# Kernel tuning notes

Measured on AMD Instinct MI355X. Metric: run time of the kernel, lower is better.

## Reference

```python
import jax, jax.numpy as jnp
import numpy as np

B, T, D, H = 1, 2049, 1024, 16
HD = D // H                      # head_dim = 64
MAX_SEQ = 1025
L = 2 * MAX_SEQ - 1              # = T (required by the module's relative shift)

def setup_inputs() -> dict:
    key = jax.random.key(0)
    ks = jax.random.split(key, 12)
    s = 0.02
    return {
        'q': jax.random.normal(ks[0], (B, T, D), dtype=jnp.float32),
        'k': jax.random.normal(ks[1], (B, T, D), dtype=jnp.float32),
        'v': jax.random.normal(ks[2], (B, T, D), dtype=jnp.float32),
        'mask': jnp.tril(jnp.ones((1, 1, T, T), dtype=jnp.int32)),  # causal
        'Wq_w': jax.random.normal(ks[3], (D, D), dtype=jnp.float32) * s,
        'Wq_b': jnp.zeros((D,), dtype=jnp.float32),
        'Wk_w': jax.random.normal(ks[4], (D, D), dtype=jnp.float32) * s,
        'Wk_b': jnp.zeros((D,), dtype=jnp.float32),
        'Wv_w': jax.random.normal(ks[5], (D, D), dtype=jnp.float32) * s,
        'Wv_b': jnp.zeros((D,), dtype=jnp.float32),
        'Er': jax.random.normal(ks[6], (L, HD), dtype=jnp.float32),
        'Wo_w': jax.random.normal(ks[7], (D, D), dtype=jnp.float32) * s,
        'Wo_b': jnp.zeros((D,), dtype=jnp.float32),
    }

def reference(q, k, v, mask, Wq_w, Wq_b, Wk_w, Wk_b, Wv_w, Wv_b, Er, Wo_w, Wo_b):
    b, t, d = q.shape
    def proj(x, w, bias):
        # nn.Linear: x @ W^T + b ; then (B,T,H,HD) -> (B,H,T,HD)
        return (x @ w.T + bias).reshape(b, t, H, HD).transpose(0, 2, 1, 3)
    qh = proj(q, Wq_w, Wq_b)
    kh = proj(k, Wk_w, Wk_b)
    vh = proj(v, Wv_w, Wv_b)
    scores = jnp.einsum('bhtd,bhsd->bhts', qh, kh)          # (B,H,T,T)
    QEr = jnp.einsum('bhtd,ld->bhtl', qh, Er)               # (B,H,T,L) with L == T
    # _relative_shift: pad a zero row on seq dim then drop first row ->
    # row i becomes QEr row i+1, last row zeros (faithful to torch code)
    rel = jnp.concatenate([QEr[:, :, 1:, :], jnp.zeros_like(QEr[:, :, :1, :])], axis=2)
    scores = scores + rel
    scores = jnp.where(mask[:, :, :t, :t] == 0, -jnp.inf, scores)
    attn = jax.nn.softmax(scores / (HD ** 0.5), axis=-1)
    ctx = jnp.einsum('bhts,bhsd->bthd', attn, vh).reshape(b, t, d)
    return ctx @ Wo_w.T + Wo_b
```

## Files before the change

### kernel.cpp

```cpp
#include <hip/hip_runtime.h>
#include <hip/hip_bf16.h>
#include <math.h>

constexpr int T_SEQ = 2049;
constexpr int D_MODEL = 1024;
constexpr int N_HEAD = 16;
constexpr int HEAD_DIM = 64;
constexpr int VT_STRIDE = 2112;
constexpr int T1_ROWS = 1152;

typedef __attribute__((ext_vector_type(8))) short short8;
typedef __attribute__((ext_vector_type(4))) short short4v;
typedef __attribute__((ext_vector_type(4))) float floatx4;

__device__ inline void load_lds16(const void* g, void* l) {
  __builtin_amdgcn_global_load_lds(
      (const __attribute__((address_space(1))) unsigned int*)g,
      (__attribute__((address_space(3))) unsigned int*)l, 16, 0, 0);
}

__device__ inline short8 cvt8_bf16(const float* p) {
  float4 a = *(const float4*)p, b = *(const float4*)(p + 4);
  __hip_bfloat16 t[8] = {__float2bfloat16(a.x), __float2bfloat16(a.y),
                         __float2bfloat16(a.z), __float2bfloat16(a.w),
                         __float2bfloat16(b.x), __float2bfloat16(b.y),
                         __float2bfloat16(b.z), __float2bfloat16(b.w)};
  return *(const short8*)t;
}

__device__ inline float bf2f(__hip_bfloat16 x) { return __bfloat162float(x); }

__global__ __launch_bounds__(256) void cast_all(
    const float* __restrict__ q, const float* __restrict__ k,
    const float* __restrict__ v, const float* __restrict__ wq,
    const float* __restrict__ wk, const float* __restrict__ wv,
    const float* __restrict__ wo, __hip_bfloat16* __restrict__ qo,
    __hip_bfloat16* __restrict__ ko, __hip_bfloat16* __restrict__ vo,
    __hip_bfloat16* __restrict__ wqo, __hip_bfloat16* __restrict__ wko,
    __hip_bfloat16* __restrict__ wvo, __hip_bfloat16* __restrict__ woo) {
  const int z = blockIdx.y;
  const float* in;
  __hip_bfloat16* out;
  int n;
  switch (z) {
    case 0: in = q; out = qo; n = T_SEQ * D_MODEL; break;
    case 1: in = k; out = ko; n = T_SEQ * D_MODEL; break;
    case 2: in = v; out = vo; n = T_SEQ * D_MODEL; break;
    case 3: in = wq; out = wqo; n = D_MODEL * D_MODEL; break;
    case 4: in = wk; out = wko; n = D_MODEL * D_MODEL; break;
    case 5: in = wv; out = wvo; n = D_MODEL * D_MODEL; break;
    default: in = wo; out = woo; n = D_MODEL * D_MODEL; break;
  }
  const int i = (blockIdx.x * 256 + threadIdx.x) * 8;
  if (i + 8 > n) return;
  *(short8*)(out + i) = cvt8_bf16(in + i);
}

template <int BN, int OUTK>
__global__ __launch_bounds__(256) void mfma_gemm(
    const __hip_bfloat16* __restrict__ A0, const __hip_bfloat16* __restrict__ A1,
    const __hip_bfloat16* __restrict__ A2, const __hip_bfloat16* __restrict__ W0,
    const __hip_bfloat16* __restrict__ W1, const __hip_bfloat16* __restrict__ W2,
    const float* __restrict__ bias0, const float* __restrict__ bias1,
    const float* __restrict__ bias2, void* C0, void* C1, void* C2, int M) {
  constexpr int K = D_MODEL;
  constexpr int NT = BN / 32;
  __shared__ __align__(16) __hip_bfloat16 As[128 * 64];
  __shared__ __align__(16) __hip_bfloat16 Bs[BN * 64];

  const int z = blockIdx.z;
  const short* A = (const short*)(z == 0 ? A0 : z == 1 ? A1 : A2);
  const short* W = (const short*)(z == 0 ? W0 : z == 1 ? W1 : W2);
  const float* bias = z == 0 ? bias0 : z == 1 ? bias1 : bias2;
  void* C = z == 0 ? C0 : z == 1 ? C1 : C2;

  const int tid = threadIdx.x;
  const int wave = tid >> 6, lane = tid & 63;
  const int col = lane & 15, quad = lane >> 4;
  const int wm = wave >> 1, wn = wave & 1;
  const int m0 = blockIdx.y * 128, n0 = blockIdx.x * BN;

  const int srow = lane >> 3;
  const int sslot = lane & 7;
  const int sch = sslot ^ srow;

  floatx4 acc[4][NT];
#pragma unroll
  for (int i = 0; i < 4; i++)
#pragma unroll
    for (int j = 0; j < NT; j++) acc[i][j] = (floatx4){0.f, 0.f, 0.f, 0.f};

  for (int k0 = 0; k0 < K; k0 += 64) {
    if (k0) __syncthreads();
#pragma unroll
    for (int i = 0; i < 4; i++) {
      const int rb = (wave * 4 + i) * 8;
      const int am = min(m0 + rb + srow, M - 1);
      load_lds16(A + (size_t)am * K + k0 + sch * 8, (char*)As + rb * 128);
    }
#pragma unroll
    for (int i = 0; i < BN / 32; i++) {
      const int rb = (wave * (BN / 32) + i) * 8;
      const int bn = n0 + rb + srow;
      load_lds16(W + (size_t)bn * K + k0 + sch * 8, (char*)Bs + rb * 128);
    }
    __syncthreads();

#pragma unroll
    for (int kk = 0; kk < 2; kk++) {
      short8 af[4], bf[NT];
#pragma unroll
      for (int t = 0; t < 4; t++) {
        const int ra = wm * 64 + t * 16 + col;
        af[t] = *(const short8*)(As + ra * 64 + ((kk * 4 + quad) ^ (ra & 7)) * 8);
      }
#pragma unroll
      for (int t = 0; t < NT; t++) {
        const int rb = wn * (BN / 2) + t * 16 + col;
        bf[t] = *(const short8*)(Bs + rb * 64 + ((kk * 4 + quad) ^ (rb & 7)) * 8);
      }
#pragma unroll
      for (int mt = 0; mt < 4; mt++)
#pragma unroll
        for (int nt = 0; nt < NT; nt++)
          acc[mt][nt] = __builtin_amdgcn_mfma_f32_16x16x32_bf16(af[mt], bf[nt],
                                                                acc[mt][nt], 0, 0, 0);
    }
  }

#pragma unroll
  for (int mt = 0; mt < 4; mt++) {
#pragma unroll
    for (int r = 0; r < 4; r++) {
      const int m = m0 + wm * 64 + mt * 16 + quad * 4 + r;
      if (m >= M) continue;
#pragma unroll
      for (int nt = 0; nt < NT; nt++) {
        const int n = n0 + wn * (BN / 2) + nt * 16 + col;
        const float val = acc[mt][nt][r] + bias[n];
        if (OUTK == 0) {
          ((float*)C)[(size_t)m * D_MODEL + n] = val;
        } else {
          if (z < 2) {
            const int h = n >> 6, hd = n & 63;
            ((__hip_bfloat16*)C)[((size_t)h * T_SEQ + m) * HEAD_DIM + hd] =
                __float2bfloat16(val);
          } else {
            ((__hip_bfloat16*)C)[(size_t)m * D_MODEL + n] = __float2bfloat16(val);
          }
        }
      }
    }
  }
}

__global__ __launch_bounds__(256) void transpose_v_er(
    const __hip_bfloat16* __restrict__ vpr, __hip_bfloat16* __restrict__ vt,
    const float* __restrict__ Er, __hip_bfloat16* __restrict__ er_bf) {
  const int tid = threadIdx.x;
  if (blockIdx.y == 16) {
    const int i = (blockIdx.x * 256 + tid) * 8;
    if (i + 8 <= T_SEQ * HEAD_DIM) *(short8*)(er_bf + i) = cvt8_bf16(Er + i);
    return;
  }
  if (blockIdx.x >= 33) return;

  __shared__ __align__(16) __hip_bfloat16 tile[64][72];
  const int t0 = blockIdx.x * 64;
  const int h = blockIdx.y;
  const short* plane = (const short*)vpr;
  short* oplane = (short*)(vt + (size_t)h * HEAD_DIM * VT_STRIDE);

  for (int idx = tid; idx < 64 * 8; idx += 256) {
    const int row = idx >> 3, ch = idx & 7;
    const int t = t0 + row;
    short8 v = {0, 0, 0, 0, 0, 0, 0, 0};
    if (t < T_SEQ) v = *(const short8*)(plane + (size_t)t * D_MODEL + h * 64 + ch * 8);
    *(short8*)&tile[row][ch * 8] = v;
  }
  __syncthreads();
  for (int idx = tid; idx < 64 * 8; idx += 256) {
    const int d = idx >> 3, ch = idx & 7;
    short8 v;
#pragma unroll
    for (int i = 0; i < 8; i++) v[i] = *(const short*)&tile[ch * 8 + i][d];
    *(short8*)(oplane + (size_t)d * VT_STRIDE + t0 + ch * 8) = v;
  }
}

__global__ __launch_bounds__(512, 4) void flash_attn(
    const __hip_bfloat16* __restrict__ qh, const __hip_bfloat16* __restrict__ kh,
    const __hip_bfloat16* __restrict__ er, const __hip_bfloat16* __restrict__ vt,
    __hip_bfloat16* __restrict__ ctx, __hip_bfloat16* __restrict__ O0,
    __hip_bfloat16* __restrict__ O1, float* __restrict__ l0g,
    float* __restrict__ l1g) {
  __shared__ __align__(16) __hip_bfloat16 Ks[2][64 * 128];
  __shared__ __align__(16) __hip_bfloat16 Vs[2][64 * 64];
  __shared__ __align__(16) __hip_bfloat16 Ps[8][1024];

  const int tid = threadIdx.x;
  const int h = blockIdx.y;
  const int b = blockIdx.x;

  const int qt = (b < 8) ? b : 8 + ((b - 8) >> 1);
  const int tq0 = qt * 128;
  const int jmax = min(tq0 + 127, T_SEQ - 1) >> 6;
  int j0, j1;
  bool alt;
  if (b < 8) {
    j0 = 0; j1 = jmax; alt = false;
  } else {
    const int mid = (jmax + 1) >> 1;
    alt = (b - 8) & 1;
    j0 = alt ? mid : 0;
    j1 = alt ? jmax : mid - 1;
  }

  const int wave = tid >> 6;
  const int lane = tid & 63;
  const int col = lane & 15;
  const int quad = lane >> 4;

  const short* qplane = (const short*)(qh + (size_t)h * T_SEQ * HEAD_DIM);
  const short* kplane = (const short*)(kh + (size_t)h * T_SEQ * HEAD_DIM);
  const short* eplane = (const short*)er;
  const short* vplane = (const short*)(vt + (size_t)h * HEAD_DIM * VT_STRIDE);

  const int t_abs = tq0 + wave * 16 + col;
  const int tload = min(t_abs, T_SEQ - 1);
  const bool hiz = (t_abs >= T_SEQ - 1);
  short8 aq[4];
#pragma unroll
  for (int kc = 0; kc < 4; kc++) {
    short8 v = *(const short8*)(qplane + (size_t)tload * 64 + kc * 32 + quad * 8);
    if (kc >= 2 && hiz) v = (short8){0, 0, 0, 0, 0, 0, 0, 0};
    aq[kc] = v;
  }

  floatx4 o[4];
  float l_lane = 0.f;
#pragma unroll
  for (int i = 0; i < 4; i++) o[i] = (floatx4){0.f, 0.f, 0.f, 0.f};

  const int tstrip = tq0 + wave * 16;
  __hip_bfloat16* psw = &Ps[wave][0];

#define STAGE_TILE(JJ, BUF)                                                        \
  {                                                                                \
    const int s0_ = (JJ) * 64;                                                     \
    _Pragma("unroll") for (int ii = 0; ii < 2; ii++) {                             \
      const int i_ = wave * 2 + ii;                                                \
      const int r_ = i_ * 4 + (lane >> 4);                                         \
      const int sl_ = lane & 15;                                                   \
      const int g_ = (sl_ & 8) | ((sl_ ^ (r_ & 7)) & 7);                           \
      const int s_ = min(s0_ + r_, T_SEQ - 1);                                     \
      const short* src_ = (g_ < 8) ? (kplane + (size_t)s_ * 64 + g_ * 8)           \
                                   : (eplane + (size_t)s_ * 64 + (g_ - 8) * 8);    \
      load_lds16(src_, (char*)&Ks[BUF][0] + i_ * 1024);                            \
    }                                                                              \
    {                                                                              \
      const int d_ = wave * 8 + (lane >> 3);                                       \
      const int sl_ = lane & 7;                                                    \
      const int g_ = sl_ ^ (d_ & 7);                                               \
      load_lds16(vplane + (size_t)d_ * VT_STRIDE + s0_ + g_ * 8,                   \
                 (char*)&Vs[BUF][0] + wave * 1024);                                \
    }                                                                              \
  }

  STAGE_TILE(j0, 0)
  int buf = 0;

  for (int j = j0; j <= j1; ++j, buf ^= 1) {
    __syncthreads();
    if (j < j1) STAGE_TILE(j + 1, buf ^ 1)

    const int s0 = j * 64;
    if (s0 > tstrip + 15) continue;

    const __hip_bfloat16* ks = &Ks[buf][0];
    const __hip_bfloat16* vs = &Vs[buf][0];

    floatx4 sacc[4];
#pragma unroll
    for (int st = 0; st < 4; st++) {
      floatx4 c = {0.f, 0.f, 0.f, 0.f};
      const int row = st * 16 + col;
#pragma unroll
      for (int kc = 0; kc < 4; kc++) {
        const int ch = kc * 4 + quad;
        const int slot = (ch & 8) | ((ch ^ (row & 7)) & 7);
        short8 ka = *(const short8*)(ks + row * 128 + slot * 8);
        c = __builtin_amdgcn_mfma_f32_16x16x32_bf16(ka, aq[kc], c, 0, 0, 0);
      }
      sacc[st] = c;
    }

    if (s0 + 63 > tstrip) {
#pragma unroll
      for (int st = 0; st < 4; st++) {
        const int sbase = s0 + st * 16 + quad * 4;
#pragma unroll
        for (int r = 0; r < 4; r++)
          if (sbase + r > t_abs) sacc[st][r] = -INFINITY;
      }
    }

    float rs = 0.f;
#pragma unroll
    for (int st = 0; st < 4; st++)
#pragma unroll
      for (int r = 0; r < 4; r++) {
        const float p = __expf(sacc[st][r] * 0.125f);
        sacc[st][r] = p;
        rs += p;
      }
    l_lane += rs;

#pragma unroll
    for (int st = 0; st < 4; st++) {
      __hip_bfloat16 pb[4];
#pragma unroll
      for (int r = 0; r < 4; r++) pb[r] = __float2bfloat16(sacc[st][r]);
      const int kcA = st >> 1;
      const int quadA = (st & 1) * 2 + (quad >> 1);
      const int off = ((kcA * 4 + quadA) * 16 + col) * 8 + (quad & 1) * 4;
      *(short4v*)(psw + off) = *(const short4v*)pb;
    }
    short8 pa[2];
#pragma unroll
    for (int kc = 0; kc < 2; kc++)
      pa[kc] = *(const short8*)(psw + ((kc * 4 + quad) * 16 + col) * 8);

#pragma unroll
    for (int nt = 0; nt < 4; nt++) {
      const int row = nt * 16 + col;
#pragma unroll
      for (int kc = 0; kc < 2; kc++) {
        const int slot = (kc * 4 + quad) ^ (row & 7);
        short8 vb = *(const short8*)(vs + row * 64 + slot * 8);
        o[nt] = __builtin_amdgcn_mfma_f32_16x16x32_bf16(pa[kc], vb, o[nt], 0, 0, 0);
      }
    }
  }

  l_lane += __shfl_xor(l_lane, 16, 64);
  l_lane += __shfl_xor(l_lane, 32, 64);

  if (b < 8) {
    const float linv = 1.0f / l_lane;
    float linv_r[4];
#pragma unroll
    for (int r = 0; r < 4; r++) linv_r[r] = __shfl(linv, quad * 4 + r, 64);
#pragma unroll
    for (int r = 0; r < 4; r++) {
      const int t = tstrip + quad * 4 + r;
#pragma unroll
      for (int nt = 0; nt < 4; nt++)
        ctx[(size_t)t * D_MODEL + h * 64 + nt * 16 + col] =
            __float2bfloat16(o[nt][r] * linv_r[r]);
    }
  } else {
    if (lane < 16) {
      const int t = tstrip + lane;
      if (t < T_SEQ) {
        if (!alt)
          l0g[h * T1_ROWS + (t - 1024)] = l_lane;
        else
          l1g[h * T1_ROWS + (t - 1024)] = l_lane;
      }
    }
#pragma unroll
    for (int r = 0; r < 4; r++) {
      const int t = tstrip + quad * 4 + r;
      if (t < T_SEQ) {
        __hip_bfloat16* dst = (!alt ? O0 : O1) + (size_t)(t - 1024) * D_MODEL;
#pragma unroll
        for (int nt = 0; nt < 4; nt++)
          dst[h * 64 + nt * 16 + col] = __float2bfloat16(o[nt][r]);
      }
    }
  }
}

__global__ __launch_bounds__(256) void finalize(
    const __hip_bfloat16* __restrict__ O0, const __hip_bfloat16* __restrict__ O1,
    const float* __restrict__ l0g, const float* __restrict__ l1g,
    __hip_bfloat16* __restrict__ ctx) {
  const int idx = blockIdx.x * 256 + threadIdx.x;
  const int tr = idx >> 7;
  const int t = 1024 + tr;
  if (t >= T_SEQ) return;
  const int ch = idx & 127;
  const int h = ch >> 3;

  const float l = l0g[h * T1_ROWS + tr] + l1g[h * T1_ROWS + tr];
  const __hip_bfloat16* a = O0 + (size_t)tr * D_MODEL + ch * 8;
  const __hip_bfloat16* bsrc = O1 + (size_t)tr * D_MODEL + ch * 8;
  const float inv = 1.0f / l;
  __hip_bfloat16 outv[8];
#pragma unroll
  for (int i = 0; i < 8; i++)
    outv[i] = __float2bfloat16((bf2f(a[i]) + bf2f(bsrc[i])) * inv);
  *(short8*)(ctx + (size_t)t * D_MODEL + ch * 8) = *(const short8*)outv;
}

extern "C" void kernel_launch(void* const* d_in, const int* in_sizes, int n_in,
                              void* d_out, int out_size, void* d_ws, size_t ws_size,
                              hipStream_t stream) {
  const float* q = (const float*)d_in[0];
  const float* k = (const float*)d_in[1];
  const float* v = (const float*)d_in[2];
  const float* Wq_w = (const float*)d_in[4];
  const float* Wq_b = (const float*)d_in[5];
  const float* Wk_w = (const float*)d_in[6];
  const float* Wk_b = (const float*)d_in[7];
  const float* Wv_w = (const float*)d_in[8];
  const float* Wv_b = (const float*)d_in[9];
  const float* Er = (const float*)d_in[10];
  const float* Wo_w = (const float*)d_in[11];
  const float* Wo_b = (const float*)d_in[12];
  float* out = (float*)d_out;

  char* ws = (char*)d_ws;
  const size_t sz_plane = (size_t)T_SEQ * D_MODEL * 2;
  const size_t sz_w = (size_t)D_MODEL * D_MODEL * 2;
  __hip_bfloat16* qbf = (__hip_bfloat16*)ws;
  __hip_bfloat16* kbf = (__hip_bfloat16*)(ws + sz_plane);
  __hip_bfloat16* vbf = (__hip_bfloat16*)(ws + 2 * sz_plane);
  char* wbase = ws + 3 * sz_plane;
  __hip_bfloat16* wob = (__hip_bfloat16*)(wbase);
  __hip_bfloat16* wqb = (__hip_bfloat16*)(wbase + sz_w);
  __hip_bfloat16* wkb = (__hip_bfloat16*)(wbase + 2 * sz_w);
  __hip_bfloat16* wvb = (__hip_bfloat16*)(wbase + 3 * sz_w);
  char* pbase = wbase + 4 * sz_w;
  __hip_bfloat16* qpr = (__hip_bfloat16*)(pbase);
  __hip_bfloat16* kpr = (__hip_bfloat16*)(pbase + sz_plane);
  __hip_bfloat16* vpr = (__hip_bfloat16*)(pbase + 2 * sz_plane);

  const size_t sz_vt = (size_t)N_HEAD * HEAD_DIM * VT_STRIDE * 2;
  const size_t sz_er = (size_t)T_SEQ * HEAD_DIM * 2;
  const size_t sz_Op = (size_t)T1_ROWS * D_MODEL * 2;
  const size_t sz_l = (size_t)N_HEAD * T1_ROWS * 4;
  __hip_bfloat16* vt = (__hip_bfloat16*)ws;
  __hip_bfloat16* er_bf = (__hip_bfloat16*)(ws + sz_vt);
  __hip_bfloat16* O0 = (__hip_bfloat16*)(ws + sz_vt + sz_er);
  __hip_bfloat16* O1 = (__hip_bfloat16*)(ws + sz_vt + sz_er + sz_Op);
  float* l0g = (float*)(ws + sz_vt + sz_er + 2 * sz_Op);
  float* l1g = (float*)(ws + sz_vt + sz_er + 2 * sz_Op + sz_l);
  __hip_bfloat16* ctxb = (__hip_bfloat16*)(wbase + sz_w);

  const dim3 blk(256);

  cast_all<<<dim3(1025, 7), blk, 0, stream>>>(q, k, v, Wq_w, Wk_w, Wv_w, Wo_w, qbf,
                                              kbf, vbf, wqb, wkb, wvb, wob);

  mfma_gemm<128, 2><<<dim3(8, 17, 3), blk, 0, stream>>>(
      qbf, kbf, vbf, wqb, wkb, wvb, Wq_b, Wk_b, Wv_b, qpr, kpr, vpr, T_SEQ);

  transpose_v_er<<<dim3(65, 17), blk, 0, stream>>>(vpr, vt, Er, er_bf);

  flash_attn<<<dim3(26, N_HEAD), dim3(512), 0, stream>>>(qpr, kpr, er_bf, vt, ctxb,
                                                         O0, O1, l0g, l1g);

  finalize<<<dim3((1025 * 128 + 255) / 256), blk, 0, stream>>>(O0, O1, l0g, l1g, ctxb);

  mfma_gemm<64, 0><<<dim3(16, 17, 1), blk, 0, stream>>>(
      ctxb, ctxb, ctxb, wob, wob, wob, Wo_b, Wo_b, Wo_b, out, out, out, T_SEQ);
}
```

Measured before the change: 204.2 us.

## Double-buffer GEMM LDS tiles and halve M tile to raise block count

The projection GEMMs now keep two LDS stages. The next K-slice is loaded with global_load_lds while the current one feeds the MFMAs, which removes one of the two barriers per iteration. The M tile shrinks from 128 to 64 rows, doubling the grid (33 row blocks instead of 17) so more CUs are busy on the 2049-row problem. In exchange each wave does fewer MFMAs per LDS fragment load, so reuse drops and traffic to the B (weight) tile rises.

```diff
diff --git a/kernel.cpp b/kernel.cpp
--- a/kernel.cpp
+++ b/kernel.cpp
@@ -65,8 +65,8 @@
     const float* __restrict__ bias2, void* C0, void* C1, void* C2, int M) {
   constexpr int K = D_MODEL;
   constexpr int NT = BN / 32;
-  __shared__ __align__(16) __hip_bfloat16 As[128 * 64];
-  __shared__ __align__(16) __hip_bfloat16 Bs[BN * 64];
+  __shared__ __align__(16) __hip_bfloat16 As[2][64 * 64];
+  __shared__ __align__(16) __hip_bfloat16 Bs[2][BN * 64];
 
   const int z = blockIdx.z;
   const short* A = (const short*)(z == 0 ? A0 : z == 1 ? A1 : A2);
@@ -78,49 +78,58 @@
   const int wave = tid >> 6, lane = tid & 63;
   const int col = lane & 15, quad = lane >> 4;
   const int wm = wave >> 1, wn = wave & 1;
-  const int m0 = blockIdx.y * 128, n0 = blockIdx.x * BN;
+  const int m0 = blockIdx.y * 64, n0 = blockIdx.x * BN;
 
   const int srow = lane >> 3;
   const int sslot = lane & 7;
   const int sch = sslot ^ srow;
 
-  floatx4 acc[4][NT];
-#pragma unroll
-  for (int i = 0; i < 4; i++)
+  floatx4 acc[2][NT];
+#pragma unroll
+  for (int i = 0; i < 2; i++)
 #pragma unroll
     for (int j = 0; j < NT; j++) acc[i][j] = (floatx4){0.f, 0.f, 0.f, 0.f};
 
-  for (int k0 = 0; k0 < K; k0 += 64) {
-    if (k0) __syncthreads();
-#pragma unroll
-    for (int i = 0; i < 4; i++) {
-      const int rb = (wave * 4 + i) * 8;
-      const int am = min(m0 + rb + srow, M - 1);
-      load_lds16(A + (size_t)am * K + k0 + sch * 8, (char*)As + rb * 128);
-    }
-#pragma unroll
-    for (int i = 0; i < BN / 32; i++) {
-      const int rb = (wave * (BN / 32) + i) * 8;
-      const int bn = n0 + rb + srow;
-      load_lds16(W + (size_t)bn * K + k0 + sch * 8, (char*)Bs + rb * 128);
-    }
+#define GSTAGE(K0, BUF)                                                     \
+  {                                                                         \
+    _Pragma("unroll") for (int ii = 0; ii < 2; ii++) {                      \
+      const int rb = (wave * 2 + ii) * 8;                                   \
+      const int am = min(m0 + rb + srow, M - 1);                            \
+      load_lds16(A + (size_t)am * K + (K0) + sch * 8,                       \
+                 (char*)&As[BUF][0] + rb * 128);                            \
+    }                                                                       \
+    _Pragma("unroll") for (int ii = 0; ii < BN / 32; ii++) {                \
+      const int rb = (wave * (BN / 32) + ii) * 8;                           \
+      const int bn = n0 + rb + srow;                                        \
+      load_lds16(W + (size_t)bn * K + (K0) + sch * 8,                       \
+                 (char*)&Bs[BUF][0] + rb * 128);                            \
+    }                                                                       \
+  }
+
+  GSTAGE(0, 0)
+  int buf = 0;
+
+  for (int kb = 0; kb < K / 64; ++kb, buf ^= 1) {
     __syncthreads();
-
+    if (kb + 1 < K / 64) GSTAGE((kb + 1) * 64, buf ^ 1)
+
+    const __hip_bfloat16* as = &As[buf][0];
+    const __hip_bfloat16* bs = &Bs[buf][0];
 #pragma unroll
     for (int kk = 0; kk < 2; kk++) {
-      short8 af[4], bf[NT];
-#pragma unroll
-      for (int t = 0; t < 4; t++) {
-        const int ra = wm * 64 + t * 16 + col;
-        af[t] = *(const short8*)(As + ra * 64 + ((kk * 4 + quad) ^ (ra & 7)) * 8);
+      short8 af[2], bf[NT];
+#pragma unroll
+      for (int t = 0; t < 2; t++) {
+        const int ra = wm * 32 + t * 16 + col;
+        af[t] = *(const short8*)(as + ra * 64 + ((kk * 4 + quad) ^ (ra & 7)) * 8);
       }
 #pragma unroll
       for (int t = 0; t < NT; t++) {
         const int rb = wn * (BN / 2) + t * 16 + col;
-        bf[t] = *(const short8*)(Bs + rb * 64 + ((kk * 4 + quad) ^ (rb & 7)) * 8);
-      }
-#pragma unroll
-      for (int mt = 0; mt < 4; mt++)
+        bf[t] = *(const short8*)(bs + rb * 64 + ((kk * 4 + quad) ^ (rb & 7)) * 8);
+      }
+#pragma unroll
+      for (int mt = 0; mt < 2; mt++)
 #pragma unroll
         for (int nt = 0; nt < NT; nt++)
           acc[mt][nt] = __builtin_amdgcn_mfma_f32_16x16x32_bf16(af[mt], bf[nt],
@@ -129,10 +138,10 @@
   }
 
 #pragma unroll
-  for (int mt = 0; mt < 4; mt++) {
+  for (int mt = 0; mt < 2; mt++) {
 #pragma unroll
     for (int r = 0; r < 4; r++) {
-      const int m = m0 + wm * 64 + mt * 16 + quad * 4 + r;
+      const int m = m0 + wm * 32 + mt * 16 + quad * 4 + r;
       if (m >= M) continue;
 #pragma unroll
       for (int nt = 0; nt < NT; nt++) {
@@ -454,7 +463,7 @@
   cast_all<<<dim3(1025, 7), blk, 0, stream>>>(q, k, v, Wq_w, Wk_w, Wv_w, Wo_w, qbf,
                                               kbf, vbf, wqb, wkb, wvb, wob);
 
-  mfma_gemm<128, 2><<<dim3(8, 17, 3), blk, 0, stream>>>(
+  mfma_gemm<128, 2><<<dim3(8, 33, 3), blk, 0, stream>>>(
       qbf, kbf, vbf, wqb, wkb, wvb, Wq_b, Wk_b, Wv_b, qpr, kpr, vpr, T_SEQ);
 
   transpose_v_er<<<dim3(65, 17), blk, 0, stream>>>(vpr, vt, Er, er_bf);
@@ -464,6 +473,6 @@
 
   finalize<<<dim3((1025 * 128 + 255) / 256), blk, 0, stream>>>(O0, O1, l0g, l1g, ctxb);
 
-  mfma_gemm<64, 0><<<dim3(16, 17, 1), blk, 0, stream>>>(
+  mfma_gemm<64, 0><<<dim3(16, 33, 1), blk, 0, stream>>>(
       ctxb, ctxb, ctxb, wob, wob, wob, Wo_b, Wo_b, Wo_b, out, out, out, T_SEQ);
 }
```

Result: slower. 208.6 us (+2.1%).
